# Kernel optimization log

Measured on AMD Instinct MI355X. Metric: run time of the kernel, lower is better.

The kernel has to match this reference:

```python
import jax, jax.numpy as jnp
import numpy as np

B, S, H, NH = 2, 2048, 1024, 16
DK = H // NH


def setup_inputs() -> dict:
    key = jax.random.key(0)
    ks = jax.random.split(key, 11)
    sc = 1.0 / np.sqrt(H)
    return {
        "q": jax.random.normal(ks[0], (B, S, H), jnp.float32),
        "v": jax.random.normal(ks[1], (B, S, H), jnp.float32),
        "k": jax.random.normal(ks[2], (B, S, H), jnp.float32),
        "Wq": jax.random.normal(ks[3], (H, H), jnp.float32) * sc,
        "bq": jax.random.normal(ks[4], (H,), jnp.float32) * 0.01,
        "Wk": jax.random.normal(ks[5], (H, H), jnp.float32) * sc,
        "bk": jax.random.normal(ks[6], (H,), jnp.float32) * 0.01,
        "Wv": jax.random.normal(ks[7], (H, H), jnp.float32) * sc,
        "bv": jax.random.normal(ks[8], (H,), jnp.float32) * 0.01,
        "Wo": jax.random.normal(ks[9], (H, H), jnp.float32) * sc,
        "bo": jax.random.normal(ks[10], (H,), jnp.float32) * 0.01,
    }


def reference(q, v, k, Wq, bq, Wk, bk, Wv, bv, Wo, bo):
    b, s, h = q.shape
    # projections; torch Linear computes x @ W.T + b
    qh = (q @ Wq.T + bq).reshape(b, s, NH, DK).transpose(0, 2, 1, 3)  # [B,NH,S,DK]
    kh = (k @ Wk.T + bk).reshape(b, s, NH, DK).transpose(0, 2, 1, 3)
    vh = (v @ Wv.T + bv).reshape(b, s, NH, DK).transpose(0, 2, 1, 3)
    scores = jnp.einsum("bhqd,bhkd->bhqk", qh, kh) / jnp.sqrt(
        jnp.asarray(DK, qh.dtype))  # [B,NH,S,S]
    probs = jax.nn.softmax(scores, axis=-1)
    ctx = jnp.einsum("bhqk,bhkd->bhqd", probs, vh)  # [B,NH,S,DK]
    concat = ctx.transpose(0, 2, 1, 3).reshape(b, s, h)
    return concat @ Wo.T + bo
```

## Files before the change

kernel.cpp:

```cpp
#include <hip/hip_runtime.h>
#include <cstddef>
#include <cstdint>

typedef _Float16 f16x8 __attribute__((ext_vector_type(8)));
typedef _Float16 f16x4 __attribute__((ext_vector_type(4)));
typedef __fp16   h16x2 __attribute__((ext_vector_type(2)));
typedef float    f32x4 __attribute__((ext_vector_type(4)));

constexpr int B_  = 2;
constexpr int S_  = 2048;
constexpr int H_  = 1024;
constexpr int NH_ = 16;
constexpr int DK_ = 64;
constexpr int M_  = B_ * S_;
constexpr int K_  = H_;

constexpr float SOFF = 4.0f;

#define MFMA32(a, b, c) __builtin_amdgcn_mfma_f32_16x16x32_f16((a), (b), (c), 0, 0, 0)
#define MFMA16(a, b, c) __builtin_amdgcn_mfma_f32_16x16x16f16((a), (b), (c), 0, 0, 0)

__device__ __forceinline__ void glds16(const void* g, void* l) {
    __builtin_amdgcn_global_load_lds(
        (const __attribute__((address_space(1))) void*)g,
        (__attribute__((address_space(3))) void*)l, 16, 0, 0);
}

__device__ __forceinline__ void pk2(f16x4& dst, int half, float a, float b) {
    const h16x2 r = __builtin_amdgcn_cvt_pkrtz(a, b);
    reinterpret_cast<h16x2*>(&dst)[half] = r;
}

struct CvtArgs {
    const float* s[7];
    _Float16*    d[7];
    int          n[7];
};

__global__ __launch_bounds__(256) void cvt7(CvtArgs a)
{
    const int seg = blockIdx.y;
    const int i = (blockIdx.x * 256 + threadIdx.x) * 8;
    if (i + 8 <= a.n[seg]) {
        const float4 v0 = *reinterpret_cast<const float4*>(a.s[seg] + i);
        const float4 v1 = *reinterpret_cast<const float4*>(a.s[seg] + i + 4);
        f16x8 o;
        o[0] = (_Float16)v0.x; o[1] = (_Float16)v0.y;
        o[2] = (_Float16)v0.z; o[3] = (_Float16)v0.w;
        o[4] = (_Float16)v1.x; o[5] = (_Float16)v1.y;
        o[6] = (_Float16)v1.z; o[7] = (_Float16)v1.w;
        *reinterpret_cast<f16x8*>(a.d[seg] + i) = o;
    }
}

struct QkvArgs {
    const _Float16* A[3];
    const _Float16* W[3];
    const float*    bias[3];
    _Float16* dstQ;
    _Float16* dstK;
    _Float16* dstV;
    float qscale;
};

__global__ __launch_bounds__(256) void gemm_qkv(QkvArgs args)
{
    constexpr int BM = 128, BN = 128, BK = 32;
    __shared__ __align__(16) _Float16 sm[8192];
    auto As = reinterpret_cast<_Float16(*)[BK]>(sm);
    auto Ws = reinterpret_cast<_Float16(*)[BK]>(sm + 4096);
    auto Tr = reinterpret_cast<_Float16(*)[64]>(sm);

    const int z = blockIdx.z;
    const _Float16* __restrict__ A = args.A[z];
    const _Float16* __restrict__ W = args.W[z];
    const float* __restrict__ bias = args.bias[z];

    const int t = threadIdx.x;
    const int w = t >> 6, lane = t & 63, quad = lane >> 4, l16 = lane & 15;
    const int m0 = blockIdx.y * BM;
    const int n0 = blockIdx.x * BN;
    const int wr = (w & 1) * 64, wc = (w >> 1) * 64;
    const int srow = lane >> 2, scol = (lane & 3) * 8;

    f32x4 acc[4][4];
#pragma unroll
    for (int i = 0; i < 4; ++i)
#pragma unroll
        for (int j = 0; j < 4; ++j) acc[i][j] = (f32x4){0.f, 0.f, 0.f, 0.f};

    for (int k0 = 0; k0 < K_; k0 += BK) {
        glds16(&A[(size_t)(m0 + w * 32 + srow) * K_ + k0 + scol], &As[w * 32][0]);
        glds16(&A[(size_t)(m0 + w * 32 + 16 + srow) * K_ + k0 + scol], &As[w * 32 + 16][0]);
        glds16(&W[(size_t)(n0 + w * 32 + srow) * K_ + k0 + scol], &Ws[w * 32][0]);
        glds16(&W[(size_t)(n0 + w * 32 + 16 + srow) * K_ + k0 + scol], &Ws[w * 32 + 16][0]);
        __syncthreads();

        f16x8 af[4], bf[4];
#pragma unroll
        for (int i = 0; i < 4; ++i)
            af[i] = *reinterpret_cast<const f16x8*>(&As[wr + i * 16 + l16][quad * 8]);
#pragma unroll
        for (int j = 0; j < 4; ++j)
            bf[j] = *reinterpret_cast<const f16x8*>(&Ws[wc + j * 16 + l16][quad * 8]);
#pragma unroll
        for (int i = 0; i < 4; ++i)
#pragma unroll
            for (int j = 0; j < 4; ++j)
                acc[i][j] = MFMA32(af[i], bf[j], acc[i][j]);
        __syncthreads();
    }

    const float scale = (z == 0) ? args.qscale : 1.0f;
    float bv[4];
#pragma unroll
    for (int j = 0; j < 4; ++j) bv[j] = bias[n0 + wc + j * 16 + l16];

    if (z == 2) {
#pragma unroll
        for (int i = 0; i < 4; ++i) {
            const int sb = m0 + wr + i * 16 + quad * 4;
            const int b = sb >> 11, s = sb & (S_ - 1);
#pragma unroll
            for (int j = 0; j < 4; ++j) {
                const int d = wc + j * 16 + l16;
                const int h = blockIdx.x * 2 + (d >> 6);
                const int dd = d & 63;
                const int kt = s >> 4, dt = dd >> 4;
                f16x4 ov;
#pragma unroll
                for (int r = 0; r < 4; ++r) ov[r] = (_Float16)(acc[i][j][r] + bv[j]);
                _Float16* base = args.dstV +
                    ((((size_t)b * NH_ + h) * 128 + kt) * 4 + dt) * 256;
                *reinterpret_cast<f16x4*>(&base[lane * 4]) = ov;
            }
        }
        return;
    }

    _Float16* dst = (z == 0) ? args.dstQ : args.dstK;
    const int b = m0 >> 11, s0 = m0 & (S_ - 1);
#pragma unroll
    for (int ch = 0; ch < 2; ++ch) {
        __syncthreads();
        if ((w >> 1) == ch) {
#pragma unroll
            for (int i = 0; i < 4; ++i)
#pragma unroll
                for (int j = 0; j < 4; ++j)
#pragma unroll
                    for (int r = 0; r < 4; ++r)
                        Tr[wr + i * 16 + quad * 4 + r][j * 16 + l16] =
                            (_Float16)((acc[i][j][r] + bv[j]) * scale);
        }
        __syncthreads();
        const int h = blockIdx.x * 2 + ch;
        _Float16* dbase = dst + ((size_t)(b * NH_ + h) * S_ + s0) * DK_;
#pragma unroll
        for (int p = 0; p < 4; ++p) {
            const int c = t + p * 256;
            *reinterpret_cast<f16x8*>(&dbase[c * 8]) =
                *reinterpret_cast<const f16x8*>(&Tr[c >> 3][(c & 7) * 8]);
        }
    }
}

__global__ __launch_bounds__(256) void gemm_out(
    const _Float16* __restrict__ A, const _Float16* __restrict__ W,
    const float* __restrict__ bias, float* __restrict__ out)
{
    constexpr int BM = 128, BN = 128, BK = 32;
    __shared__ _Float16 As[BM][BK];
    __shared__ _Float16 Ws[BN][BK];

    const int t = threadIdx.x;
    const int w = t >> 6, lane = t & 63, quad = lane >> 4, l16 = lane & 15;
    const int m0 = blockIdx.y * BM;
    const int n0 = blockIdx.x * BN;
    const int wr = (w & 1) * 64, wc = (w >> 1) * 64;
    const int srow = lane >> 2, scol = (lane & 3) * 8;

    f32x4 acc[4][4];
#pragma unroll
    for (int i = 0; i < 4; ++i)
#pragma unroll
        for (int j = 0; j < 4; ++j) acc[i][j] = (f32x4){0.f, 0.f, 0.f, 0.f};

    for (int k0 = 0; k0 < K_; k0 += BK) {
        glds16(&A[(size_t)(m0 + w * 32 + srow) * K_ + k0 + scol], &As[w * 32][0]);
        glds16(&A[(size_t)(m0 + w * 32 + 16 + srow) * K_ + k0 + scol], &As[w * 32 + 16][0]);
        glds16(&W[(size_t)(n0 + w * 32 + srow) * K_ + k0 + scol], &Ws[w * 32][0]);
        glds16(&W[(size_t)(n0 + w * 32 + 16 + srow) * K_ + k0 + scol], &Ws[w * 32 + 16][0]);
        __syncthreads();

        f16x8 af[4], bf[4];
#pragma unroll
        for (int i = 0; i < 4; ++i)
            af[i] = *reinterpret_cast<const f16x8*>(&As[wr + i * 16 + l16][quad * 8]);
#pragma unroll
        for (int j = 0; j < 4; ++j)
            bf[j] = *reinterpret_cast<const f16x8*>(&Ws[wc + j * 16 + l16][quad * 8]);
#pragma unroll
        for (int i = 0; i < 4; ++i)
#pragma unroll
            for (int j = 0; j < 4; ++j)
                acc[i][j] = MFMA32(af[i], bf[j], acc[i][j]);
        __syncthreads();
    }

    float bv[4];
#pragma unroll
    for (int j = 0; j < 4; ++j) bv[j] = bias[n0 + wc + j * 16 + l16];

#pragma unroll
    for (int i = 0; i < 4; ++i)
#pragma unroll
        for (int j = 0; j < 4; ++j)
#pragma unroll
            for (int r = 0; r < 4; ++r)
                out[(size_t)(m0 + wr + i * 16 + quad * 4 + r) * H_ +
                    n0 + wc + j * 16 + l16] = acc[i][j][r] + bv[j];
}

__global__ __launch_bounds__(256) void attn_mfma(
    const _Float16* __restrict__ qh, const _Float16* __restrict__ kh,
    const _Float16* __restrict__ vfrag, _Float16* __restrict__ ctx)
{
    __shared__ float Ob[4][64][36];
    __shared__ float Ls[4][64];
    __shared__ float Linv[64];

    const int t = threadIdx.x;
    const int w = t >> 6, lane = t & 63, quad = lane >> 4, l16 = lane & 15;
    const int q0 = blockIdx.x * 64;
    const int bh = blockIdx.y;

    const _Float16* qb = qh + (size_t)bh * S_ * DK_;
    const _Float16* kb = kh + (size_t)bh * S_ * DK_;
    const _Float16* vb = vfrag + (size_t)bh * 128 * 4 * 256;

    f16x8 qf[4][2];
#pragma unroll
    for (int qt = 0; qt < 4; ++qt)
#pragma unroll
        for (int h2 = 0; h2 < 2; ++h2)
            qf[qt][h2] = *reinterpret_cast<const f16x8*>(
                &qb[(size_t)(q0 + qt * 16 + l16) * DK_ + h2 * 32 + quad * 8]);

    f32x4 o[4][4];
#pragma unroll
    for (int dt = 0; dt < 4; ++dt)
#pragma unroll
        for (int qt = 0; qt < 4; ++qt) o[dt][qt] = (f32x4){0.f, 0.f, 0.f, 0.f};
    float lp_[4];
#pragma unroll
    for (int qt = 0; qt < 4; ++qt) lp_[qt] = 0.f;

    const _Float16* kptr = kb + (size_t)(w * 16 + l16) * DK_ + quad * 8;
    const _Float16* vptr = vb + (size_t)w * 4 * 256 + lane * 4;

    for (int ti = 0; ti < 32; ++ti) {
        const f16x8 kf0 = *reinterpret_cast<const f16x8*>(kptr);
        const f16x8 kf1 = *reinterpret_cast<const f16x8*>(kptr + 32);
        f16x4 vf[4];
#pragma unroll
        for (int dt = 0; dt < 4; ++dt)
            vf[dt] = *reinterpret_cast<const f16x4*>(vptr + dt * 256);
        kptr += 64 * DK_;
        vptr += 4 * 4 * 256;

        f32x4 sc[4];
#pragma unroll
        for (int qt = 0; qt < 4; ++qt) {
            sc[qt] = (f32x4){-SOFF, -SOFF, -SOFF, -SOFF};
            sc[qt] = MFMA32(kf0, qf[qt][0], sc[qt]);
            sc[qt] = MFMA32(kf1, qf[qt][1], sc[qt]);
        }

        f16x4 pf[4];
#pragma unroll
        for (int qt = 0; qt < 4; ++qt) {
            const float p0 = __builtin_amdgcn_exp2f(sc[qt][0]);
            const float p1 = __builtin_amdgcn_exp2f(sc[qt][1]);
            const float p2 = __builtin_amdgcn_exp2f(sc[qt][2]);
            const float p3 = __builtin_amdgcn_exp2f(sc[qt][3]);
            lp_[qt] += (p0 + p1) + (p2 + p3);
            f16x4 pv;
            pk2(pv, 0, p0, p1);
            pk2(pv, 1, p2, p3);
            pf[qt] = pv;
        }

#pragma unroll
        for (int dt = 0; dt < 4; ++dt)
#pragma unroll
            for (int qt = 0; qt < 4; ++qt)
                o[dt][qt] = MFMA16(vf[dt], pf[qt], o[dt][qt]);
    }

#pragma unroll
    for (int qt = 0; qt < 4; ++qt) {
        float l = lp_[qt];
        l += __shfl_xor(l, 16);
        l += __shfl_xor(l, 32);
        if (quad == 0) Ls[w][qt * 16 + l16] = l;
    }
    __syncthreads();
    if (t < 64)
        Linv[t] = 1.f / (((Ls[0][t] + Ls[1][t]) + (Ls[2][t] + Ls[3][t])));

    const int b = bh >> 4, hh = bh & 15;
    const int dg = t & 3, qq = t >> 2;
#pragma unroll
    for (int ph = 0; ph < 2; ++ph) {
        __syncthreads();
#pragma unroll
        for (int dl = 0; dl < 2; ++dl) {
            const int dt = ph * 2 + dl;
#pragma unroll
            for (int qt = 0; qt < 4; ++qt)
                *reinterpret_cast<f32x4*>(
                    &Ob[w][qt * 16 + l16][dl * 16 + quad * 4]) = o[dt][qt];
        }
        __syncthreads();
        f32x4 s0 = (f32x4){0.f, 0.f, 0.f, 0.f};
        f32x4 s1 = (f32x4){0.f, 0.f, 0.f, 0.f};
#pragma unroll
        for (int ww = 0; ww < 4; ++ww) {
            s0 += *reinterpret_cast<const f32x4*>(&Ob[ww][qq][dg * 8]);
            s1 += *reinterpret_cast<const f32x4*>(&Ob[ww][qq][dg * 8 + 4]);
        }
        const float li = Linv[qq];
        f16x8 ov;
#pragma unroll
        for (int r = 0; r < 4; ++r) {
            ov[r]     = (_Float16)(s0[r] * li);
            ov[4 + r] = (_Float16)(s1[r] * li);
        }
        *reinterpret_cast<f16x8*>(
            &ctx[((size_t)b * S_ + q0 + qq) * H_ + hh * 64 + ph * 32 + dg * 8]) = ov;
    }
}

extern "C" void kernel_launch(void* const* d_in, const int* in_sizes, int n_in,
                              void* d_out, int out_size, void* d_ws,
                              size_t ws_size, hipStream_t stream)
{
    (void)in_sizes; (void)n_in; (void)out_size; (void)ws_size;
    const float* q  = (const float*)d_in[0];
    const float* v  = (const float*)d_in[1];
    const float* k  = (const float*)d_in[2];
    const float* Wq = (const float*)d_in[3];
    const float* bq = (const float*)d_in[4];
    const float* Wk = (const float*)d_in[5];
    const float* bk = (const float*)d_in[6];
    const float* Wv = (const float*)d_in[7];
    const float* bv = (const float*)d_in[8];
    const float* Wo = (const float*)d_in[9];
    const float* bo = (const float*)d_in[10];
    float* out = (float*)d_out;

    constexpr size_t NACT = (size_t)M_ * K_;
    constexpr size_t NW   = (size_t)H_ * H_;
    _Float16* p = (_Float16*)d_ws;
    _Float16* q16  = p;
    _Float16* k16  = p + NACT;
    _Float16* v16  = p + 2 * NACT;
    _Float16* w16q = p + 3 * NACT;
    _Float16* w16k = w16q + NW;
    _Float16* w16v = w16k + NW;
    _Float16* w16o = w16v + NW;
    _Float16* qhd  = w16o + NW;
    _Float16* khd  = qhd + NACT;
    _Float16* vfr  = khd + NACT;
    _Float16* ctx  = q16;

    CvtArgs ca;
    ca.s[0] = q;  ca.d[0] = q16;  ca.n[0] = (int)NACT;
    ca.s[1] = v;  ca.d[1] = v16;  ca.n[1] = (int)NACT;
    ca.s[2] = k;  ca.d[2] = k16;  ca.n[2] = (int)NACT;
    ca.s[3] = Wq; ca.d[3] = w16q; ca.n[3] = (int)NW;
    ca.s[4] = Wk; ca.d[4] = w16k; ca.n[4] = (int)NW;
    ca.s[5] = Wv; ca.d[5] = w16v; ca.n[5] = (int)NW;
    ca.s[6] = Wo; ca.d[6] = w16o; ca.n[6] = (int)NW;
    cvt7<<<dim3(2048, 7), 256, 0, stream>>>(ca);

    QkvArgs ga;
    ga.A[0] = q16;  ga.W[0] = w16q; ga.bias[0] = bq;
    ga.A[1] = k16;  ga.W[1] = w16k; ga.bias[1] = bk;
    ga.A[2] = v16;  ga.W[2] = w16v; ga.bias[2] = bv;
    ga.dstQ = qhd;  ga.dstK = khd;  ga.dstV = vfr;
    ga.qscale = 0.125f * 1.4426950408889634f;

    gemm_qkv<<<dim3(H_ / 128, M_ / 128, 3), 256, 0, stream>>>(ga);

    attn_mfma<<<dim3(S_ / 64, B_ * NH_), 256, 0, stream>>>(qhd, khd, vfr, ctx);

    gemm_out<<<dim3(H_ / 128, M_ / 128), 256, 0, stream>>>(ctx, w16o, bo, out);
}
```

Measured before the change: 237.3 us.

## Fuse fp32-to-fp16 conversion into GEMM tile loads, drop separate convert kernel

Removes the standalone cvt7 kernel, which converted all activations and weights to fp16 in a separate pass. The QKV and output GEMMs now read fp32 straight from global memory, convert in registers, and store fp16 into LDS. This saves one launch and a full fp16 write-and-reread of the inputs. In exchange, each GEMM reads twice as many bytes per tile, and weights are re-read and re-converted by every M-block. The async global_load_lds path for those operands is replaced by synchronous register loads, which may expose more latency.

```diff
diff --git a/kernel.cpp b/kernel.cpp
--- a/kernel.cpp
+++ b/kernel.cpp
@@ -31,32 +31,21 @@
     reinterpret_cast<h16x2*>(&dst)[half] = r;
 }
 
-struct CvtArgs {
-    const float* s[7];
-    _Float16*    d[7];
-    int          n[7];
-};
-
-__global__ __launch_bounds__(256) void cvt7(CvtArgs a)
-{
-    const int seg = blockIdx.y;
-    const int i = (blockIdx.x * 256 + threadIdx.x) * 8;
-    if (i + 8 <= a.n[seg]) {
-        const float4 v0 = *reinterpret_cast<const float4*>(a.s[seg] + i);
-        const float4 v1 = *reinterpret_cast<const float4*>(a.s[seg] + i + 4);
-        f16x8 o;
-        o[0] = (_Float16)v0.x; o[1] = (_Float16)v0.y;
-        o[2] = (_Float16)v0.z; o[3] = (_Float16)v0.w;
-        o[4] = (_Float16)v1.x; o[5] = (_Float16)v1.y;
-        o[6] = (_Float16)v1.z; o[7] = (_Float16)v1.w;
-        *reinterpret_cast<f16x8*>(a.d[seg] + i) = o;
-    }
+__device__ __forceinline__ f16x8 cvt8(const float* src) {
+    const float4 u0 = *reinterpret_cast<const float4*>(src);
+    const float4 u1 = *reinterpret_cast<const float4*>(src + 4);
+    f16x8 o;
+    o[0] = (_Float16)u0.x; o[1] = (_Float16)u0.y;
+    o[2] = (_Float16)u0.z; o[3] = (_Float16)u0.w;
+    o[4] = (_Float16)u1.x; o[5] = (_Float16)u1.y;
+    o[6] = (_Float16)u1.z; o[7] = (_Float16)u1.w;
+    return o;
 }
 
 struct QkvArgs {
-    const _Float16* A[3];
-    const _Float16* W[3];
-    const float*    bias[3];
+    const float* A[3];
+    const float* W[3];
+    const float* bias[3];
     _Float16* dstQ;
     _Float16* dstK;
     _Float16* dstV;
@@ -72,9 +61,112 @@
     auto Tr = reinterpret_cast<_Float16(*)[64]>(sm);
 
     const int z = blockIdx.z;
-    const _Float16* __restrict__ A = args.A[z];
-    const _Float16* __restrict__ W = args.W[z];
+    const float* __restrict__ A = args.A[z];
+    const float* __restrict__ W = args.W[z];
     const float* __restrict__ bias = args.bias[z];
+
+    const int t = threadIdx.x;
+    const int w = t >> 6, lane = t & 63, quad = lane >> 4, l16 = lane & 15;
+    const int m0 = blockIdx.y * BM;
+    const int n0 = blockIdx.x * BN;
+    const int wr = (w & 1) * 64, wc = (w >> 1) * 64;
+
+    const int r0c = t >> 2, c0c = (t & 3) * 8;
+    const int r1c = (t + 256) >> 2, c1c = c0c;
+
+    f32x4 acc[4][4];
+#pragma unroll
+    for (int i = 0; i < 4; ++i)
+#pragma unroll
+        for (int j = 0; j < 4; ++j) acc[i][j] = (f32x4){0.f, 0.f, 0.f, 0.f};
+
+    for (int k0 = 0; k0 < K_; k0 += BK) {
+        *reinterpret_cast<f16x8*>(&As[r0c][c0c]) =
+            cvt8(&A[(size_t)(m0 + r0c) * K_ + k0 + c0c]);
+        *reinterpret_cast<f16x8*>(&As[r1c][c1c]) =
+            cvt8(&A[(size_t)(m0 + r1c) * K_ + k0 + c1c]);
+        *reinterpret_cast<f16x8*>(&Ws[r0c][c0c]) =
+            cvt8(&W[(size_t)(n0 + r0c) * K_ + k0 + c0c]);
+        *reinterpret_cast<f16x8*>(&Ws[r1c][c1c]) =
+            cvt8(&W[(size_t)(n0 + r1c) * K_ + k0 + c1c]);
+        __syncthreads();
+
+        f16x8 af[4], bf[4];
+#pragma unroll
+        for (int i = 0; i < 4; ++i)
+            af[i] = *reinterpret_cast<const f16x8*>(&As[wr + i * 16 + l16][quad * 8]);
+#pragma unroll
+        for (int j = 0; j < 4; ++j)
+            bf[j] = *reinterpret_cast<const f16x8*>(&Ws[wc + j * 16 + l16][quad * 8]);
+#pragma unroll
+        for (int i = 0; i < 4; ++i)
+#pragma unroll
+            for (int j = 0; j < 4; ++j)
+                acc[i][j] = MFMA32(af[i], bf[j], acc[i][j]);
+        __syncthreads();
+    }
+
+    const float scale = (z == 0) ? args.qscale : 1.0f;
+    float bv[4];
+#pragma unroll
+    for (int j = 0; j < 4; ++j) bv[j] = bias[n0 + wc + j * 16 + l16];
+
+    if (z == 2) {
+#pragma unroll
+        for (int i = 0; i < 4; ++i) {
+            const int sb = m0 + wr + i * 16 + quad * 4;
+            const int b = sb >> 11, s = sb & (S_ - 1);
+#pragma unroll
+            for (int j = 0; j < 4; ++j) {
+                const int d = wc + j * 16 + l16;
+                const int h = blockIdx.x * 2 + (d >> 6);
+                const int dd = d & 63;
+                const int kt = s >> 4, dt = dd >> 4;
+                f16x4 ov;
+#pragma unroll
+                for (int r = 0; r < 4; ++r) ov[r] = (_Float16)(acc[i][j][r] + bv[j]);
+                _Float16* base = args.dstV +
+                    ((((size_t)b * NH_ + h) * 128 + kt) * 4 + dt) * 256;
+                *reinterpret_cast<f16x4*>(&base[lane * 4]) = ov;
+            }
+        }
+        return;
+    }
+
+    _Float16* dst = (z == 0) ? args.dstQ : args.dstK;
+    const int b = m0 >> 11, s0 = m0 & (S_ - 1);
+#pragma unroll
+    for (int ch = 0; ch < 2; ++ch) {
+        __syncthreads();
+        if ((w >> 1) == ch) {
+#pragma unroll
+            for (int i = 0; i < 4; ++i)
+#pragma unroll
+                for (int j = 0; j < 4; ++j)
+#pragma unroll
+                    for (int r = 0; r < 4; ++r)
+                        Tr[wr + i * 16 + quad * 4 + r][j * 16 + l16] =
+                            (_Float16)((acc[i][j][r] + bv[j]) * scale);
+        }
+        __syncthreads();
+        const int h = blockIdx.x * 2 + ch;
+        _Float16* dbase = dst + ((size_t)(b * NH_ + h) * S_ + s0) * DK_;
+#pragma unroll
+        for (int p = 0; p < 4; ++p) {
+            const int c = t + p * 256;
+            *reinterpret_cast<f16x8*>(&dbase[c * 8]) =
+                *reinterpret_cast<const f16x8*>(&Tr[c >> 3][(c & 7) * 8]);
+        }
+    }
+}
+
+__global__ __launch_bounds__(256) void gemm_out(
+    const _Float16* __restrict__ A, const float* __restrict__ W,
+    const float* __restrict__ bias, float* __restrict__ out)
+{
+    constexpr int BM = 128, BN = 128, BK = 32;
+    __shared__ _Float16 As[BM][BK];
+    __shared__ _Float16 Ws[BN][BK];
 
     const int t = threadIdx.x;
     const int w = t >> 6, lane = t & 63, quad = lane >> 4, l16 = lane & 15;
@@ -82,6 +174,8 @@
     const int n0 = blockIdx.x * BN;
     const int wr = (w & 1) * 64, wc = (w >> 1) * 64;
     const int srow = lane >> 2, scol = (lane & 3) * 8;
+    const int r0c = t >> 2, c0c = (t & 3) * 8;
+    const int r1c = (t + 256) >> 2;
 
     f32x4 acc[4][4];
 #pragma unroll
@@ -92,105 +186,10 @@
     for (int k0 = 0; k0 < K_; k0 += BK) {
         glds16(&A[(size_t)(m0 + w * 32 + srow) * K_ + k0 + scol], &As[w * 32][0]);
         glds16(&A[(size_t)(m0 + w * 32 + 16 + srow) * K_ + k0 + scol], &As[w * 32 + 16][0]);
-        glds16(&W[(size_t)(n0 + w * 32 + srow) * K_ + k0 + scol], &Ws[w * 32][0]);
-        glds16(&W[(size_t)(n0 + w * 32 + 16 + srow) * K_ + k0 + scol], &Ws[w * 32 + 16][0]);
-        __syncthreads();
-
-        f16x8 af[4], bf[4];
-#pragma unroll
-        for (int i = 0; i < 4; ++i)
-            af[i] = *reinterpret_cast<const f16x8*>(&As[wr + i * 16 + l16][quad * 8]);
-#pragma unroll
-        for (int j = 0; j < 4; ++j)
-            bf[j] = *reinterpret_cast<const f16x8*>(&Ws[wc + j * 16 + l16][quad * 8]);
-#pragma unroll
-        for (int i = 0; i < 4; ++i)
-#pragma unroll
-            for (int j = 0; j < 4; ++j)
-                acc[i][j] = MFMA32(af[i], bf[j], acc[i][j]);
-        __syncthreads();
-    }
-
-    const float scale = (z == 0) ? args.qscale : 1.0f;
-    float bv[4];
-#pragma unroll
-    for (int j = 0; j < 4; ++j) bv[j] = bias[n0 + wc + j * 16 + l16];
-
-    if (z == 2) {
-#pragma unroll
-        for (int i = 0; i < 4; ++i) {
-            const int sb = m0 + wr + i * 16 + quad * 4;
-            const int b = sb >> 11, s = sb & (S_ - 1);
-#pragma unroll
-            for (int j = 0; j < 4; ++j) {
-                const int d = wc + j * 16 + l16;
-                const int h = blockIdx.x * 2 + (d >> 6);
-                const int dd = d & 63;
-                const int kt = s >> 4, dt = dd >> 4;
-                f16x4 ov;
-#pragma unroll
-                for (int r = 0; r < 4; ++r) ov[r] = (_Float16)(acc[i][j][r] + bv[j]);
-                _Float16* base = args.dstV +
-                    ((((size_t)b * NH_ + h) * 128 + kt) * 4 + dt) * 256;
-                *reinterpret_cast<f16x4*>(&base[lane * 4]) = ov;
-            }
-        }
-        return;
-    }
-
-    _Float16* dst = (z == 0) ? args.dstQ : args.dstK;
-    const int b = m0 >> 11, s0 = m0 & (S_ - 1);
-#pragma unroll
-    for (int ch = 0; ch < 2; ++ch) {
-        __syncthreads();
-        if ((w >> 1) == ch) {
-#pragma unroll
-            for (int i = 0; i < 4; ++i)
-#pragma unroll
-                for (int j = 0; j < 4; ++j)
-#pragma unroll
-                    for (int r = 0; r < 4; ++r)
-                        Tr[wr + i * 16 + quad * 4 + r][j * 16 + l16] =
-                            (_Float16)((acc[i][j][r] + bv[j]) * scale);
-        }
-        __syncthreads();
-        const int h = blockIdx.x * 2 + ch;
-        _Float16* dbase = dst + ((size_t)(b * NH_ + h) * S_ + s0) * DK_;
-#pragma unroll
-        for (int p = 0; p < 4; ++p) {
-            const int c = t + p * 256;
-            *reinterpret_cast<f16x8*>(&dbase[c * 8]) =
-                *reinterpret_cast<const f16x8*>(&Tr[c >> 3][(c & 7) * 8]);
-        }
-    }
-}
-
-__global__ __launch_bounds__(256) void gemm_out(
-    const _Float16* __restrict__ A, const _Float16* __restrict__ W,
-    const float* __restrict__ bias, float* __restrict__ out)
-{
-    constexpr int BM = 128, BN = 128, BK = 32;
-    __shared__ _Float16 As[BM][BK];
-    __shared__ _Float16 Ws[BN][BK];
-
-    const int t = threadIdx.x;
-    const int w = t >> 6, lane = t & 63, quad = lane >> 4, l16 = lane & 15;
-    const int m0 = blockIdx.y * BM;
-    const int n0 = blockIdx.x * BN;
-    const int wr = (w & 1) * 64, wc = (w >> 1) * 64;
-    const int srow = lane >> 2, scol = (lane & 3) * 8;
-
-    f32x4 acc[4][4];
-#pragma unroll
-    for (int i = 0; i < 4; ++i)
-#pragma unroll
-        for (int j = 0; j < 4; ++j) acc[i][j] = (f32x4){0.f, 0.f, 0.f, 0.f};
-
-    for (int k0 = 0; k0 < K_; k0 += BK) {
-        glds16(&A[(size_t)(m0 + w * 32 + srow) * K_ + k0 + scol], &As[w * 32][0]);
-        glds16(&A[(size_t)(m0 + w * 32 + 16 + srow) * K_ + k0 + scol], &As[w * 32 + 16][0]);
-        glds16(&W[(size_t)(n0 + w * 32 + srow) * K_ + k0 + scol], &Ws[w * 32][0]);
-        glds16(&W[(size_t)(n0 + w * 32 + 16 + srow) * K_ + k0 + scol], &Ws[w * 32 + 16][0]);
+        *reinterpret_cast<f16x8*>(&Ws[r0c][c0c]) =
+            cvt8(&W[(size_t)(n0 + r0c) * K_ + k0 + c0c]);
+        *reinterpret_cast<f16x8*>(&Ws[r1c][c0c]) =
+            cvt8(&W[(size_t)(n0 + r1c) * K_ + k0 + c0c]);
         __syncthreads();
 
         f16x8 af[4], bf[4];
@@ -361,34 +360,16 @@
     float* out = (float*)d_out;
 
     constexpr size_t NACT = (size_t)M_ * K_;
-    constexpr size_t NW   = (size_t)H_ * H_;
     _Float16* p = (_Float16*)d_ws;
-    _Float16* q16  = p;
-    _Float16* k16  = p + NACT;
-    _Float16* v16  = p + 2 * NACT;
-    _Float16* w16q = p + 3 * NACT;
-    _Float16* w16k = w16q + NW;
-    _Float16* w16v = w16k + NW;
-    _Float16* w16o = w16v + NW;
-    _Float16* qhd  = w16o + NW;
-    _Float16* khd  = qhd + NACT;
-    _Float16* vfr  = khd + NACT;
-    _Float16* ctx  = q16;
-
-    CvtArgs ca;
-    ca.s[0] = q;  ca.d[0] = q16;  ca.n[0] = (int)NACT;
-    ca.s[1] = v;  ca.d[1] = v16;  ca.n[1] = (int)NACT;
-    ca.s[2] = k;  ca.d[2] = k16;  ca.n[2] = (int)NACT;
-    ca.s[3] = Wq; ca.d[3] = w16q; ca.n[3] = (int)NW;
-    ca.s[4] = Wk; ca.d[4] = w16k; ca.n[4] = (int)NW;
-    ca.s[5] = Wv; ca.d[5] = w16v; ca.n[5] = (int)NW;
-    ca.s[6] = Wo; ca.d[6] = w16o; ca.n[6] = (int)NW;
-    cvt7<<<dim3(2048, 7), 256, 0, stream>>>(ca);
+    _Float16* qhd = p;
+    _Float16* khd = qhd + NACT;
+    _Float16* vfr = khd + NACT;
+    _Float16* ctx = vfr + NACT;
 
     QkvArgs ga;
-    ga.A[0] = q16;  ga.W[0] = w16q; ga.bias[0] = bq;
-    ga.A[1] = k16;  ga.W[1] = w16k; ga.bias[1] = bk;
-    ga.A[2] = v16;  ga.W[2] = w16v; ga.bias[2] = bv;
+    ga.A[0] = q;  ga.W[0] = Wq; ga.bias[0] = bq;
+    ga.A[1] = k;  ga.W[1] = Wk; ga.bias[1] = bk;
+    ga.A[2] = v;  ga.W[2] = Wv; ga.bias[2] = bv;
     ga.dstQ = qhd;  ga.dstK = khd;  ga.dstV = vfr;
     ga.qscale = 0.125f * 1.4426950408889634f;
 
@@ -396,5 +377,5 @@
 
     attn_mfma<<<dim3(S_ / 64, B_ * NH_), 256, 0, stream>>>(qhd, khd, vfr, ctx);
 
-    gemm_out<<<dim3(H_ / 128, M_ / 128), 256, 0, stream>>>(ctx, w16o, bo, out);
-}
+    gemm_out<<<dim3(H_ / 128, M_ / 128), 256, 0, stream>>>(ctx, Wo, bo, out);
+}
```

Measured after the change: 268.7 us. 13.2% more time.
